# Kernel optimization log

Measured on AMD Instinct MI355X. Metric: run time of the kernel, lower is better.

The kernel has to match this reference:

```python
import jax, jax.numpy as jnp
import numpy as np

N_QUBITS = 11
N_LAYERS = 4
N_FEATURES = 8
N_SAMPLES = 16
MEAS_QUBITS = (0, 1, 2, 3)
DIM = 2 ** N_QUBITS


def _cnot_matrix(control, target, n):
    # Faithful to get_single_CNOT_matrix: qubit 0 is the MOST significant bit
    # (bin(i).zfill(n) indexing). Column i maps to row with target bit flipped
    # when control bit is 1.
    idx = np.arange(2 ** n)
    ctrl = (idx >> (n - 1 - control)) & 1
    rows = np.where(ctrl == 1, idx ^ (1 << (n - 1 - target)), idx)
    u = np.zeros((2 ** n, 2 ** n), np.float32)
    u[rows, idx] = 1.0
    return jnp.asarray(u, jnp.complex64)


def _get_angles(X, weights, biases):
    # X: (B, F) -> angles (B, L, Q, 3), tiling features with repetition
    B, F = X.shape
    n_angles = N_QUBITS * N_LAYERS * 3
    reps = n_angles // F + 1
    Xe = jnp.tile(X, (1, reps))[:, :n_angles].reshape(B, N_LAYERS, N_QUBITS, 3)
    return Xe * weights[None] + biases[None]


def _single_qubit_unitaries(ang):
    # ang: (B, Q, 3) = (phi, theta, omega)  ->  (B, Q, 2, 2) complex Rot gates
    phi, theta, omega = ang[..., 0], ang[..., 1], ang[..., 2]
    ct = jnp.cos(theta / 2)
    st = jnp.sin(theta / 2)
    po = (phi + omega) / 2
    pm = (phi - omega) / 2
    m00 = jnp.exp(-1j * po) * ct
    m01 = -jnp.exp(1j * pm) * st
    m10 = jnp.exp(-1j * pm) * st
    m11 = jnp.exp(1j * po) * ct
    M = jnp.stack([m00, m01, m10, m11], axis=-1)
    return M.reshape(ang.shape[0], ang.shape[1], 2, 2).astype(jnp.complex64)


def _system_unitary(M):
    # Sequential Kronecker product over qubits (qubit 0 = leftmost factor),
    # identical math to the source's einsum-based kron: (B, 2^n, 2^n).
    B = M.shape[0]
    U = M[:, 0]
    for q in range(1, N_QUBITS):
        d = U.shape[1]
        U = (U[:, :, None, :, None] * M[:, q][:, None, :, None, :]).reshape(B, d * 2, d * 2)
    return U


def setup_inputs() -> dict:
    key = jax.random.key(0)
    k1, k2, k3 = jax.random.split(key, 3)
    X = jax.random.normal(k1, (N_SAMPLES, N_FEATURES), jnp.float32)
    weights = jax.random.uniform(k2, (N_LAYERS, N_QUBITS, 3), jnp.float32)
    biases = jax.random.uniform(k3, (N_LAYERS, N_QUBITS, 3), jnp.float32)
    return {"X": X, "weights": weights, "biases": biases}


def reference(X, weights, biases):
    B = X.shape[0]
    angles = _get_angles(X, weights, biases)  # (B, L, Q, 3)
    state = jnp.zeros((B, DIM), jnp.complex64).at[:, 0].set(1.0)
    ring = [(i, i + 1) for i in range(N_QUBITS - 1)] + [(N_QUBITS - 1, 0)]
    cnots = [_cnot_matrix(c, t, N_QUBITS) for c, t in ring]
    for l in range(N_LAYERS):
        U = _system_unitary(_single_qubit_unitaries(angles[:, l]))  # (B, D, D)
        state = jnp.einsum('aij,aj->ai', U, state)
        for Uc in cnots:
            state = jnp.einsum('ij,aj->ai', Uc, state)
    probs = jnp.abs(state) ** 2  # (B, D) float32
    idx = jnp.arange(DIM)
    outs = [jnp.sum(probs * (1.0 - 2.0 * ((idx >> (N_QUBITS - 1 - q)) & 1)).astype(probs.dtype), axis=1)
            for q in MEAS_QUBITS]
    return jnp.stack(outs, axis=1)  # (B, n_meas)
```

## Files before the change

### kernel.cpp

```cpp
#include <hip/hip_runtime.h>

#define NQ 11
#define NL 4
#define NF 8
#define DIM 2048
#define NGATES (NL * NQ)

__host__ __device__ constexpr int ring_perm(int y) {
    int z = y ^ ((y & 1) << 10);
    for (int k = 10; k >= 1; --k)
        z ^= ((z >> (11 - k)) & 1) << (10 - k);
    return z;
}

__device__ __forceinline__ int swz(int i) { return i ^ ((i >> 5) & 31); }

__device__ __forceinline__ void wave_sync() { __builtin_amdgcn_wave_barrier(); }

__device__ __forceinline__ float2 cmul(float2 a, float2 b) {
    return make_float2(a.x * b.x - a.y * b.y, a.x * b.y + a.y * b.x);
}

__device__ __forceinline__ void rot_pair(float2& a, float2& c,
                                         const float4 M0, const float4 M1) {
    float2 na, nc;
    na.x = M0.x * a.x - M0.y * a.y + M0.z * c.x - M0.w * c.y;
    na.y = M0.x * a.y + M0.y * a.x + M0.z * c.y + M0.w * c.x;
    nc.x = M1.x * a.x - M1.y * a.y + M1.z * c.x - M1.w * c.y;
    nc.y = M1.x * a.y + M1.y * a.x + M1.z * c.y + M1.w * c.x;
    a = na; c = nc;
}

template<int P2, int P1, int P0, bool PERM>
__device__ __forceinline__ void group3(const float2* __restrict__ src,
                                       float2* __restrict__ dst,
                                       const float (*gm)[8], int g, int base) {
    constexpr int E2 = 1 << P2, E1 = 1 << P1, E0 = 1 << P0;
    constexpr int K2 = PERM ? ring_perm(1 << P2) : (1 << P2);
    constexpr int K1 = PERM ? ring_perm(1 << P1) : (1 << P1);
    constexpr int K0 = PERM ? ring_perm(1 << P0) : (1 << P0);

    const float4* mA = (const float4*)gm[g];
    const float4* mB = (const float4*)gm[g + 1];
    const float4* mC = (const float4*)gm[g + 2];
    const float4 A0 = mA[0], A1 = mA[1];
    const float4 B0 = mB[0], B1 = mB[1];
    const float4 C0 = mC[0], C1 = mC[1];

    const int rb = PERM ? ring_perm(base) : base;
    float2 s[8];
#pragma unroll
    for (int k = 0; k < 8; ++k) {
        const int idx = rb ^ ((k & 4) ? K2 : 0) ^ ((k & 2) ? K1 : 0) ^ ((k & 1) ? K0 : 0);
        s[k] = src[swz(idx)];
    }
    rot_pair(s[0], s[4], A0, A1); rot_pair(s[1], s[5], A0, A1);
    rot_pair(s[2], s[6], A0, A1); rot_pair(s[3], s[7], A0, A1);
    rot_pair(s[0], s[2], B0, B1); rot_pair(s[1], s[3], B0, B1);
    rot_pair(s[4], s[6], B0, B1); rot_pair(s[5], s[7], B0, B1);
    rot_pair(s[0], s[1], C0, C1); rot_pair(s[2], s[3], C0, C1);
    rot_pair(s[4], s[5], C0, C1); rot_pair(s[6], s[7], C0, C1);
#pragma unroll
    for (int k = 0; k < 8; ++k) {
        const int a = base | ((k & 4) ? E2 : 0) | ((k & 2) ? E1 : 0) | ((k & 1) ? E0 : 0);
        dst[swz(a)] = s[k];
    }
}

__device__ __forceinline__ void group2q(float2* buf, const float (*gm)[8],
                                        int g, int t) {
    const float4* mB = (const float4*)gm[g];
    const float4* mC = (const float4*)gm[g + 1];
    const float4 B0 = mB[0], B1 = mB[1];
    const float4 C0 = mC[0], C1 = mC[1];
#pragma unroll
    for (int j = 0; j < 2; ++j) {
        const int base = (t << 3) | (j << 2);
        float2 s[4];
#pragma unroll
        for (int k = 0; k < 4; ++k) s[k] = buf[swz(base | k)];
        rot_pair(s[0], s[2], B0, B1); rot_pair(s[1], s[3], B0, B1);
        rot_pair(s[0], s[1], C0, C1); rot_pair(s[2], s[3], C0, C1);
#pragma unroll
        for (int k = 0; k < 4; ++k) buf[swz(base | k)] = s[k];
    }
}

__device__ __forceinline__ void group2q_meas(const float2* __restrict__ buf,
                                             const float (*gm)[8], int g, int t,
                                             float v[4]) {
    const float4* mB = (const float4*)gm[g];
    const float4* mC = (const float4*)gm[g + 1];
    const float4 B0 = mB[0], B1 = mB[1];
    const float4 C0 = mC[0], C1 = mC[1];
    const int tb = t << 3;
    const int p0 = __popc(tb & 0x3FF) & 1;
    const int p1 = __popc(tb & 0x600) & 1;
    const int p2 = __popc(tb & 0x700) & 1;
    const int p3 = __popc(tb & 0x780) & 1;
    float Psum = 0.f, Aalt = 0.f;
#pragma unroll
    for (int j = 0; j < 2; ++j) {
        const int base = tb | (j << 2);
        float2 s[4];
#pragma unroll
        for (int k = 0; k < 4; ++k) s[k] = buf[swz(base | k)];
        rot_pair(s[0], s[2], B0, B1); rot_pair(s[1], s[3], B0, B1);
        rot_pair(s[0], s[1], C0, C1); rot_pair(s[2], s[3], C0, C1);
#pragma unroll
        for (int k = 0; k < 4; ++k) {
            const float p = s[k].x * s[k].x + s[k].y * s[k].y;
            Psum += p;
            Aalt += (__popc((j << 2) | k) & 1) ? -p : p;
        }
    }
    v[0] = p0 ? -Aalt : Aalt;
    v[1] = p1 ? -Psum : Psum;
    v[2] = p2 ? -Psum : Psum;
    v[3] = p3 ? -Psum : Psum;
}

__global__ __launch_bounds__(256)
void qsim_kernel(const float* __restrict__ X, const float* __restrict__ W,
                 const float* __restrict__ Bi, float* __restrict__ out)
{
    __shared__ float2 bufA[DIM];
    __shared__ float2 bufB[DIM];
    __shared__ __align__(16) float gm[NGATES][8];
    __shared__ float sc[192][2];
    __shared__ float red[4][4];

    const int b = blockIdx.x;
    const int t = threadIdx.x;

    {
        const int sl = t & 63;
        const int g = 21 * (t >> 6) + sl / 3;
        const int c = sl % 3;
        if (sl < 63 && g < NGATES) {
            const int base = g * 3;
            const float x0 = X[b * NF + ((base + 0) & 7)];
            const float x1 = X[b * NF + ((base + 1) & 7)];
            const float x2 = X[b * NF + ((base + 2) & 7)];
            const float phi   = x0 * W[base + 0] + Bi[base + 0];
            const float theta = x1 * W[base + 1] + Bi[base + 1];
            const float omega = x2 * W[base + 2] + Bi[base + 2];
            const float arg = (c == 0) ? 0.5f * theta
                            : (c == 1) ? 0.5f * (phi + omega)
                                       : 0.5f * (phi - omega);
            float s_, c_; sincosf(arg, &s_, &c_);
            sc[t][0] = s_; sc[t][1] = c_;
        }
        wave_sync();
        if (sl < 63 && g < NGATES && c == 0) {
            const float sh  = sc[t][0],     ch  = sc[t][1];
            const float spo = sc[t + 1][0], cpo = sc[t + 1][1];
            const float spm = sc[t + 2][0], cpm = sc[t + 2][1];
            gm[g][0] =  cpo * ch;  gm[g][1] = -spo * ch;
            gm[g][2] = -cpm * sh;  gm[g][3] = -spm * sh;
            gm[g][4] =  cpm * sh;  gm[g][5] = -spm * sh;
            gm[g][6] =  cpo * ch;  gm[g][7] =  spo * ch;
        }
    }
    __syncthreads();

    float2* S = bufA;
    float2* T = bufB;

    {
        float2 c0[11], c1[11];
#pragma unroll
        for (int q = 0; q < 11; ++q) {
            c0[q] = make_float2(gm[q][0], gm[q][1]);
            c1[q] = make_float2(gm[q][4], gm[q][5]);
        }
        float2 P = ((t >> 0) & 1) ? c1[10] : c0[10];
#pragma unroll
        for (int bbit = 1; bbit < 8; ++bbit)
            P = cmul(P, ((t >> bbit) & 1) ? c1[10 - bbit] : c0[10 - bbit]);
        float2 t2[4];
        t2[0] = cmul(c0[1], c0[0]);
        t2[1] = cmul(c1[1], c0[0]);
        t2[2] = cmul(c0[1], c1[0]);
        t2[3] = cmul(c1[1], c1[0]);
#pragma unroll
        for (int k = 0; k < 8; ++k) {
            const float2 h = cmul((k & 1) ? c1[2] : c0[2], t2[k >> 1]);
            S[swz(t + 256 * k)] = cmul(P, h);
        }
    }
    __syncthreads();

#pragma unroll
    for (int l = 1; l < NL; ++l) {
        group3<10, 9, 8, true>(S, T, gm, l * NQ + 0, t); { float2* x = S; S = T; T = x; }
        __syncthreads();
        const int base765 = ((t >> 5) << 8) | (t & 31);
        const int base432 = ((t >> 2) << 5) | (t & 3);
        group3<7, 6, 5, false>(S, S, gm, l * NQ + 3, base765);  wave_sync();
        group3<4, 3, 2, false>(S, S, gm, l * NQ + 6, base432);  wave_sync();
        if (l < NL - 1) {
            group2q(S, gm, l * NQ + 9, t);
            __syncthreads();
        }
    }

    float v[4];
    group2q_meas(S, gm, (NL - 1) * NQ + 9, t, v);

#pragma unroll
    for (int q = 0; q < 4; ++q)
#pragma unroll
        for (int off = 32; off >= 1; off >>= 1)
            v[q] += __shfl_down(v[q], off, 64);
    if ((t & 63) == 0) {
#pragma unroll
        for (int q = 0; q < 4; ++q) red[t >> 6][q] = v[q];
    }
    __syncthreads();
    if (t < 4) {
        out[b * 4 + t] = red[0][t] + red[1][t] + red[2][t] + red[3][t];
    }
}

extern "C" void kernel_launch(void* const* d_in, const int* in_sizes, int n_in,
                              void* d_out, int out_size, void* d_ws, size_t ws_size,
                              hipStream_t stream) {
    const float* X  = (const float*)d_in[0];
    const float* W  = (const float*)d_in[1];
    const float* Bi = (const float*)d_in[2];
    float* out = (float*)d_out;
    qsim_kernel<<<16, 256, 0, stream>>>(X, W, Bi, out);
}
```

Measured before the change: 65.05 us.

## Fold first layer-1 gates into register-built product state and drop an initial barrier

Each wave now redundantly computes sines and cosines for the layer-0 gates and the first two layer-1 gates, so it can build the product state in registers without waiting on a block-wide barrier after gate-matrix setup. The product-state amplitudes are generated directly in the ring-permuted order, and layer-1 qubits 0 and 1 are applied in registers before the first shared write. The rest of layer 1 then runs as three in-place wave-local group passes, which removes one permuting buffer swap and its barrier. The cost is extra redundant trig and register work per wave, plus more complex index bookkeeping.

```diff
diff --git a/kernel.cpp b/kernel.cpp
--- a/kernel.cpp
+++ b/kernel.cpp
@@ -127,17 +127,23 @@
     __shared__ float2 bufA[DIM];
     __shared__ float2 bufB[DIM];
     __shared__ __align__(16) float gm[NGATES][8];
-    __shared__ float sc[192][2];
+    __shared__ float sc[4][64][2];
     __shared__ float red[4][4];
 
     const int b = blockIdx.x;
     const int t = threadIdx.x;
+    const int w = t >> 6, ln = t & 63;
 
     {
-        const int sl = t & 63;
-        const int g = 21 * (t >> 6) + sl / 3;
-        const int c = sl % 3;
-        if (sl < 63 && g < NGATES) {
+        int g = -1, c = 0;
+        if (ln < 33)      { g = ln / 3;                 c = ln - 3 * g; }
+        else if (ln < 39) { const int u = ln - 33; g = 11 + u / 3; c = u - 3 * (u / 3); }
+        else {
+            const int g0 = 13 + 8 * w, ng = (w == 3) ? 7 : 8;
+            const int u = ln - 39;
+            if (u < 3 * ng) { g = g0 + u / 3; c = u - 3 * (u / 3); }
+        }
+        if (g >= 0) {
             const int base = g * 3;
             const float x0 = X[b * NF + ((base + 0) & 7)];
             const float x1 = X[b * NF + ((base + 1) & 7)];
@@ -149,50 +155,96 @@
                             : (c == 1) ? 0.5f * (phi + omega)
                                        : 0.5f * (phi - omega);
             float s_, c_; sincosf(arg, &s_, &c_);
-            sc[t][0] = s_; sc[t][1] = c_;
+            sc[w][ln][0] = s_; sc[w][ln][1] = c_;
         }
         wave_sync();
-        if (sl < 63 && g < NGATES && c == 0) {
-            const float sh  = sc[t][0],     ch  = sc[t][1];
-            const float spo = sc[t + 1][0], cpo = sc[t + 1][1];
-            const float spm = sc[t + 2][0], cpm = sc[t + 2][1];
+        if (g >= 13 && c == 0) {
+            const float sh  = sc[w][ln][0],     ch  = sc[w][ln][1];
+            const float spo = sc[w][ln + 1][0], cpo = sc[w][ln + 1][1];
+            const float spm = sc[w][ln + 2][0], cpm = sc[w][ln + 2][1];
             gm[g][0] =  cpo * ch;  gm[g][1] = -spo * ch;
             gm[g][2] = -cpm * sh;  gm[g][3] = -spm * sh;
             gm[g][4] =  cpm * sh;  gm[g][5] = -spm * sh;
             gm[g][6] =  cpo * ch;  gm[g][7] =  spo * ch;
         }
     }
-    __syncthreads();
 
     float2* S = bufA;
     float2* T = bufB;
 
     {
+        float4 A0, A1, B0, B1;
+        {
+            const float sh  = sc[w][33][0], ch  = sc[w][33][1];
+            const float spo = sc[w][34][0], cpo = sc[w][34][1];
+            const float spm = sc[w][35][0], cpm = sc[w][35][1];
+            A0 = make_float4(cpo * ch, -spo * ch, -cpm * sh, -spm * sh);
+            A1 = make_float4(cpm * sh, -spm * sh,  cpo * ch,  spo * ch);
+        }
+        {
+            const float sh  = sc[w][36][0], ch  = sc[w][36][1];
+            const float spo = sc[w][37][0], cpo = sc[w][37][1];
+            const float spm = sc[w][38][0], cpm = sc[w][38][1];
+            B0 = make_float4(cpo * ch, -spo * ch, -cpm * sh, -spm * sh);
+            B1 = make_float4(cpm * sh, -spm * sh,  cpo * ch,  spo * ch);
+        }
         float2 c0[11], c1[11];
 #pragma unroll
         for (int q = 0; q < 11; ++q) {
-            c0[q] = make_float2(gm[q][0], gm[q][1]);
-            c1[q] = make_float2(gm[q][4], gm[q][5]);
-        }
-        float2 P = ((t >> 0) & 1) ? c1[10] : c0[10];
-#pragma unroll
-        for (int bbit = 1; bbit < 8; ++bbit)
-            P = cmul(P, ((t >> bbit) & 1) ? c1[10 - bbit] : c0[10 - bbit]);
-        float2 t2[4];
-        t2[0] = cmul(c0[1], c0[0]);
-        t2[1] = cmul(c1[1], c0[0]);
-        t2[2] = cmul(c0[1], c1[0]);
-        t2[3] = cmul(c1[1], c1[0]);
+            const float sh  = sc[w][3 * q][0],     ch  = sc[w][3 * q][1];
+            const float spo = sc[w][3 * q + 1][0], cpo = sc[w][3 * q + 1][1];
+            const float spm = sc[w][3 * q + 2][0], cpm = sc[w][3 * q + 2][1];
+            c0[q] = make_float2(cpo * ch, -spo * ch);
+            c1[q] = make_float2(cpm * sh, -spm * sh);
+        }
+        constexpr int K2 = ring_perm(1 << 10);
+        constexpr int K1 = ring_perm(1 << 9);
+        constexpr int K0 = ring_perm(1 << 8);
+        static_assert(((K2 | K1 | K0) & ~0x780) == 0,
+                      "gather deltas must be confined to bits 10..7");
+        const int rb = ring_perm(t);
+        float2 F = ((rb >> 6) & 1) ? c1[4] : c0[4];
+#pragma unroll
+        for (int q = 5; q < 11; ++q)
+            F = cmul(F, ((rb >> (10 - q)) & 1) ? c1[q] : c0[q]);
+        float2 Q01[4], Q23[4], G[4];
+#pragma unroll
+        for (int i = 0; i < 4; ++i) {
+            Q01[i] = cmul((i & 2) ? c1[0] : c0[0], (i & 1) ? c1[1] : c0[1]);
+            Q23[i] = cmul((i & 2) ? c1[2] : c0[2], (i & 1) ? c1[3] : c0[3]);
+        }
+#pragma unroll
+        for (int i = 0; i < 4; ++i) G[i] = cmul(F, Q01[i]);
+        float2 s[8];
 #pragma unroll
         for (int k = 0; k < 8; ++k) {
-            const float2 h = cmul((k & 1) ? c1[2] : c0[2], t2[k >> 1]);
-            S[swz(t + 256 * k)] = cmul(P, h);
+            const int y = rb ^ ((k & 4) ? K2 : 0) ^ ((k & 2) ? K1 : 0) ^ ((k & 1) ? K0 : 0);
+            s[k] = cmul(G[(y >> 9) & 3], Q23[(y >> 7) & 3]);
+        }
+        rot_pair(s[0], s[4], A0, A1); rot_pair(s[1], s[5], A0, A1);
+        rot_pair(s[2], s[6], A0, A1); rot_pair(s[3], s[7], A0, A1);
+        rot_pair(s[0], s[2], B0, B1); rot_pair(s[1], s[3], B0, B1);
+        rot_pair(s[4], s[6], B0, B1); rot_pair(s[5], s[7], B0, B1);
+#pragma unroll
+        for (int k = 0; k < 8; ++k) {
+            const int a = t | ((k & 4) ? 1024 : 0) | ((k & 2) ? 512 : 0) | ((k & 1) ? 256 : 0);
+            S[swz(a)] = s[k];
         }
     }
     __syncthreads();
 
-#pragma unroll
-    for (int l = 1; l < NL; ++l) {
+    {
+        const int base86  = ((t >> 6) << 9) | (t & 63);
+        const int base543 = ((t >> 6) << 9) | (((t >> 3) & 7) << 6) | (t & 7);
+        const int base210 = ((t >> 6) << 9) | ((t & 63) << 3);
+        group3<8, 7, 6, false>(S, S, gm, 13, base86);  wave_sync();
+        group3<5, 4, 3, false>(S, S, gm, 16, base543); wave_sync();
+        group3<2, 1, 0, false>(S, S, gm, 19, base210);
+    }
+    __syncthreads();
+
+#pragma unroll
+    for (int l = 2; l < NL; ++l) {
         group3<10, 9, 8, true>(S, T, gm, l * NQ + 0, t); { float2* x = S; S = T; T = x; }
         __syncthreads();
         const int base765 = ((t >> 5) << 8) | (t & 31);
```

Measured after the change: 66.39 us. 2.1% more time.
